# Kernel optimization log

Measured on AMD Instinct MI355X. Metric: run time of the kernel, lower is better.

The kernel has to match this reference:

```python
import jax, jax.numpy as jnp
import numpy as np

B, S, D = 2, 2048, 2048
H, KVH = 16, 4
HD = D // H  # 128


def _rope_angles(seq, head_dim):
    theta = 1.0 / (10000.0 ** (jnp.arange(0, head_dim, 2, dtype=jnp.float32) / head_dim))
    ang = jnp.arange(seq, dtype=jnp.float32)[:, None] * theta[None, :]  # [S, HD/2]
    return jnp.cos(ang), jnp.sin(ang)


def _apply_rotary(t, cos, sin):
    # t: [B, S, h, HD]; pairs are (even, odd) along last dim (view_as_complex semantics)
    tr = t[..., 0::2]
    ti = t[..., 1::2]
    c = cos[None, :, None, :]
    s = sin[None, :, None, :]
    out_r = tr * c - ti * s
    out_i = tr * s + ti * c
    return jnp.stack([out_r, out_i], axis=-1).reshape(t.shape)


def setup_inputs() -> dict:
    key = jax.random.key(0)
    ks = jax.random.split(key, 8)
    sd = 1.0 / np.sqrt(D)
    return {
        'x': jax.random.normal(ks[0], (B, S, D), dtype=jnp.float32),
        'wq': jax.random.normal(ks[1], (D, D), dtype=jnp.float32) * sd,
        'bq': jax.random.normal(ks[2], (D,), dtype=jnp.float32) * 0.01,
        'wk': jax.random.normal(ks[3], (D, KVH * HD), dtype=jnp.float32) * sd,
        'bk': jax.random.normal(ks[4], (KVH * HD,), dtype=jnp.float32) * 0.01,
        'wv': jax.random.normal(ks[5], (D, KVH * HD), dtype=jnp.float32) * sd,
        'bv': jax.random.normal(ks[6], (KVH * HD,), dtype=jnp.float32) * 0.01,
        'wo': jax.random.normal(ks[7], (D, D), dtype=jnp.float32) * sd,
    }


def reference(x, wq, bq, wk, bk, wv, bv, wo):
    b, s, d = x.shape
    q = (x @ wq + bq).reshape(b, s, H, HD)
    k = (x @ wk + bk).reshape(b, s, KVH, HD)
    v = (x @ wv + bv).reshape(b, s, KVH, HD)

    cos, sin = _rope_angles(s, HD)
    q = _apply_rotary(q, cos, sin)
    k = _apply_rotary(k, cos, sin)

    repeat = H // KVH
    k = jnp.repeat(k, repeat, axis=2)  # [B, S, H, HD]
    v = jnp.repeat(v, repeat, axis=2)

    scale = 1.0 / np.sqrt(HD)
    att_score = jnp.einsum('bqhd,bkhd->bqhk', q, k) * scale  # [B, S, H, S]
    att_weight = jax.nn.softmax(att_score, axis=-1)
    out = jnp.einsum('bqhk,bkhd->bqhd', att_weight, v)
    out = out.reshape(b, s, H * HD)
    return out @ wo
```

## Files before the change

### kernel.cpp

```cpp
#include <hip/hip_runtime.h>
#include <hip/hip_bf16.h>
#include <cstdint>

typedef __attribute__((ext_vector_type(4))) float f32x4;
typedef __attribute__((ext_vector_type(16))) float f32x16;
typedef __attribute__((ext_vector_type(8))) short bf16x8;
typedef __attribute__((ext_vector_type(4))) unsigned int u32x4;
typedef unsigned short u16;
typedef unsigned int u32;

__device__ __forceinline__ u16 f2b(float x) {
  __hip_bfloat16 h = __float2bfloat16(x);
  return *reinterpret_cast<u16*>(&h);
}

__device__ __forceinline__ u32 pk(float a, float b) {
  __hip_bfloat162 h2 = __float22bfloat162_rn(float2{a, b});
  return *reinterpret_cast<u32*>(&h2);
}

__device__ __forceinline__ void gload16(const void* g, void* l) {
  __builtin_amdgcn_global_load_lds((const __attribute__((address_space(1))) u32*)g,
                                   (__attribute__((address_space(3))) u32*)l, 16, 0, 0);
}

__device__ __forceinline__ float xmax32(float x) {
  return fmaxf(x, __shfl_xor(x, 32, 64));
}
__device__ __forceinline__ float xsum32(float x) {
  return x + __shfl_xor(x, 32, 64);
}


__global__ void cvt_f32_bf16(const float* __restrict__ in, u16* __restrict__ out, int n4) {
  int idx = (blockIdx.x * 256 + threadIdx.x);
  if (idx < n4) {
    const float4 v = *(const float4*)(in + (size_t)idx * 4);
    u16* o = out + (size_t)idx * 4;
    o[0] = f2b(v.x); o[1] = f2b(v.y); o[2] = f2b(v.z); o[3] = f2b(v.w);
  }
}

__global__ void w_transpose_cvt(const float* __restrict__ w0, const float* __restrict__ w1,
                                const float* __restrict__ w2, int b0, int b1,
                                int N0, int N1, int N2,
                                u16* __restrict__ out, int K) {
  __shared__ float tile[32][33];
  int k0 = blockIdx.x * 32, n0 = blockIdx.y * 32;
  const float* src; int srcN; int c0;
  if (n0 < b0)      { src = w0; srcN = N0; c0 = n0; }
  else if (n0 < b1) { src = w1; srcN = N1; c0 = n0 - b0; }
  else              { src = w2; srcN = N2; c0 = n0 - b1; }
  int tx = threadIdx.x & 31, ty = threadIdx.x >> 5;
#pragma unroll
  for (int j = 0; j < 32; j += 8)
    tile[ty + j][tx] = src[(size_t)(k0 + ty + j) * srcN + c0 + tx];
  __syncthreads();
#pragma unroll
  for (int j = 0; j < 32; j += 8)
    out[(size_t)(n0 + ty + j) * K + k0 + tx] = f2b(tile[tx][ty + j]);
}

__global__ void pack_bias(const float* __restrict__ bq, const float* __restrict__ bk,
                          const float* __restrict__ bv, float* __restrict__ out) {
  int i = blockIdx.x * 256 + threadIdx.x;
  if (i < 3072) out[i] = (i < 2048) ? bq[i] : ((i < 2560) ? bk[i - 2048] : bv[i - 2560]);
}

__global__ void v_transpose_cvt(const float* __restrict__ qkv, u16* __restrict__ vt) {
  __shared__ float tile[32][33];
  int s0 = blockIdx.x * 32;
  int d0 = blockIdx.y * 32;
  int z = blockIdx.z;
  int b = z >> 2, kvh = z & 3;
  int tx = threadIdx.x & 31, ty = threadIdx.x >> 5;
#pragma unroll
  for (int j = 0; j < 32; j += 8)
    tile[ty + j][tx] = qkv[((size_t)(b * 2048 + s0 + ty + j)) * 3072 + 2560 + kvh * 128 + d0 + tx];
  __syncthreads();
#pragma unroll
  for (int j = 0; j < 32; j += 8)
    vt[((size_t)z * 128 + d0 + ty + j) * 2048 + s0 + tx] = f2b(tile[tx][ty + j]);
}

__global__ void rope_cvt(const float* __restrict__ qkv, u16* __restrict__ out,
                         int lognh, int col0, float scale) {
  int idx = blockIdx.x * 256 + threadIdx.x;
  int i = idx & 63;
  int nh = 1 << lognh;
  int h = (idx >> 6) & (nh - 1);
  int bs = idx >> (6 + lognh);
  int s = bs & 2047;
  int b = bs >> 11;
  const float* src = qkv + (size_t)bs * 3072 + col0 + h * 128 + 2 * i;
  float tr = src[0], ti = src[1];
  float theta = expf(-(float)i * 0.14391156831212787f);
  float ang = (float)s * theta;
  float sv, cv;
  sincosf(ang, &sv, &cv);
  float orr = (tr * cv - ti * sv) * scale;
  float oii = (tr * sv + ti * cv) * scale;
  u16* dst = out + (((size_t)(b * nh + h) * 2048 + s) * 128 + 2 * i);
  dst[0] = f2b(orr);
  dst[1] = f2b(oii);
}

__global__ __launch_bounds__(256) void gemm_bt_bf16(
    const u16* __restrict__ A, const u16* __restrict__ Bt,
    const float* __restrict__ bias, float* __restrict__ C,
    int M, int N, int K, int gx) {
  __shared__ u16 As[128 * 32];
  __shared__ u16 Bs[128 * 32];
  const int tid = threadIdx.x;
  const int lane = tid & 63;
  const int w = tid >> 6;
  const int wr = w >> 1, wc = w & 1;
  const int nb = gridDim.x;
  const int swz = (blockIdx.x & 7) * (nb >> 3) + (blockIdx.x >> 3);
  const int m0 = (swz / gx) * 128;
  const int n0 = (swz % gx) * 128;

  f32x4 acc[4][4] = {};

  for (int k0 = 0; k0 < K; k0 += 32) {
#pragma unroll
    for (int it = 0; it < 2; ++it) {
      int c = tid + it * 256;
      int row = c >> 2;
      int off = (c & 3) * 8;
      gload16(A + (size_t)(m0 + row) * K + k0 + off, (u16*)As + w * 512 + it * 2048);
      gload16(Bt + (size_t)(n0 + row) * K + k0 + off, (u16*)Bs + w * 512 + it * 2048);
    }
    __syncthreads();
    const int col8 = (lane >> 4) * 8;
    bf16x8 a[4], bfr[4];
#pragma unroll
    for (int m = 0; m < 4; ++m)
      a[m] = *(const bf16x8*)&As[(wr * 64 + m * 16 + (lane & 15)) * 32 + col8];
#pragma unroll
    for (int n = 0; n < 4; ++n)
      bfr[n] = *(const bf16x8*)&Bs[(wc * 64 + n * 16 + (lane & 15)) * 32 + col8];
#pragma unroll
    for (int m = 0; m < 4; ++m)
#pragma unroll
      for (int n = 0; n < 4; ++n)
        acc[m][n] = __builtin_amdgcn_mfma_f32_16x16x32_bf16(a[m], bfr[n], acc[m][n], 0, 0, 0);
    __syncthreads();
  }

#pragma unroll
  for (int m = 0; m < 4; ++m) {
    int row = m0 + wr * 64 + m * 16 + ((lane >> 4) << 2);
#pragma unroll
    for (int n = 0; n < 4; ++n) {
      int col = n0 + wc * 64 + n * 16 + (lane & 15);
      float bvv = bias ? bias[col] : 0.f;
      float* cp = C + (size_t)row * N + col;
#pragma unroll
      for (int r = 0; r < 4; ++r) cp[(size_t)r * N] = acc[m][n][r] + bvv;
    }
  }
}

__global__ __launch_bounds__(128, 3) void flash_attn(
    const u16* __restrict__ Qr, const u16* __restrict__ Kr,
    const u16* __restrict__ Vt, u16* __restrict__ Att) {
  __shared__ u16 Ks[2][32 * 128];
  __shared__ u16 Vs[2][128 * 32];
  const int tid = threadIdx.x, lane = tid & 63, w = tid >> 6;
  const int lo = lane & 31, hi = lane >> 5;
  const int bid = blockIdx.x;
  const int g = bid & 7;
  const int local = bid >> 3;
  const int b = g >> 2, kvh = g & 3;
  const int h = kvh * 4 + (local & 3);
  const int q0 = (local >> 2) * 64 + w * 32;

  const char* Khead = (const char*)(Kr + (size_t)(b * 4 + kvh) * 2048 * 128);
  const char* Vhead = (const char*)(Vt + (size_t)(b * 4 + kvh) * 128 * 2048);

  bf16x8 qf[8];
  {
    const u16* qp = Qr + ((size_t)(b * 16 + h) * 2048 + q0 + lo) * 128 + hi * 8;
#pragma unroll
    for (int ds = 0; ds < 8; ++ds) qf[ds] = *(const bf16x8*)(qp + ds * 16);
  }

#define STAGE(bufi, t)                                                        \
  {                                                                           \
    _Pragma("unroll")                                                         \
    for (int it = 0; it < 4; ++it) {                                          \
      int c = it * 128 + tid;                                                 \
      int krow = c >> 4;                                                      \
      int koff = krow * 256 + ((c & 15) << 4 ^ ((krow & 7) << 4));            \
      gload16(Khead + (size_t)(t) * 8192 + koff,                              \
              (u16*)Ks[bufi] + it * 1024 + w * 512);                          \
      int vrow = c >> 2;                                                      \
      int voff = vrow * 4096 + ((c & 3) << 4 ^ (((vrow >> 1) & 3) << 4));     \
      gload16(Vhead + (size_t)(t) * 64 + voff,                                \
              (u16*)Vs[bufi] + it * 1024 + w * 512);                          \
    }                                                                         \
  }

  f32x16 o0[4] = {};
  float m_run = -3.0e38f, l_run = 0.f;
  const int swz = (lo & 7) << 4;
  const int vswz = ((lo >> 1) & 3) << 4;
  const int hi16 = hi * 16;

  STAGE(0, 0);
  __syncthreads();

  int buf = 0;
  for (int t = 0; t < 64; ++t) {
    int tn = (t < 63) ? t + 1 : 63;
    STAGE(buf ^ 1, tn);

    const char* Kb = (const char*)Ks[buf];
    const char* Vb = (const char*)Vs[buf];

    f32x16 sc = {};
    __builtin_amdgcn_s_setprio(1);
#pragma unroll
    for (int ds = 0; ds < 8; ++ds) {
      bf16x8 kf = *(const bf16x8*)(Kb + lo * 256 + ((ds * 32 + hi16) ^ swz));
      sc = __builtin_amdgcn_mfma_f32_32x32x16_bf16(kf, qf[ds], sc, 0, 0, 0);
    }
    __builtin_amdgcn_s_setprio(0);

    {
      float t0 = fmaxf(fmaxf(sc[0], sc[1]), sc[2]);
      float t1 = fmaxf(fmaxf(sc[3], sc[4]), sc[5]);
      float t2 = fmaxf(fmaxf(sc[6], sc[7]), sc[8]);
      float t3 = fmaxf(fmaxf(sc[9], sc[10]), sc[11]);
      float t4 = fmaxf(fmaxf(sc[12], sc[13]), sc[14]);
      float pmax = xmax32(fmaxf(fmaxf(fmaxf(t0, t1), t2), fmaxf(fmaxf(t3, t4), sc[15])));
      if (!__all(pmax - m_run <= 11.0f)) {
        float mnew = fmaxf(m_run, pmax);
        float rs = exp2f(m_run - mnew);
        m_run = mnew;
        l_run *= rs;
#pragma unroll
        for (int r = 0; r < 16; ++r) {
          float rsr = __shfl(rs, (r & 3) + 8 * (r >> 2) + 4 * hi, 64);
          o0[0][r] *= rsr; o0[1][r] *= rsr; o0[2][r] *= rsr; o0[3][r] *= rsr;
        }
      }
      float lsum = 0.f;
#pragma unroll
      for (int r = 0; r < 16; ++r) { float p = exp2f(sc[r] - m_run); sc[r] = p; lsum += p; }
      l_run += xsum32(lsum);
    }

    bf16x8 pa0, pa1;
    {
      u32 a0 = pk(sc[0], sc[1]),   a1 = pk(sc[2], sc[3]);
      u32 b0 = pk(sc[4], sc[5]),   b1 = pk(sc[6], sc[7]);
      u32 t0 = hi ? a0 : b0, t1 = hi ? a1 : b1;
      u32 r0 = __shfl_xor(t0, 32, 64), r1 = __shfl_xor(t1, 32, 64);
      u32x4 w0;
      w0[0] = hi ? r0 : a0; w0[1] = hi ? r1 : a1;
      w0[2] = hi ? b0 : r0; w0[3] = hi ? b1 : r1;
      pa0 = __builtin_bit_cast(bf16x8, w0);
      u32 c0 = pk(sc[8], sc[9]),   c1 = pk(sc[10], sc[11]);
      u32 d0 = pk(sc[12], sc[13]), d1 = pk(sc[14], sc[15]);
      u32 t2 = hi ? c0 : d0, t3 = hi ? c1 : d1;
      u32 r2 = __shfl_xor(t2, 32, 64), r3 = __shfl_xor(t3, 32, 64);
      u32x4 w1;
      w1[0] = hi ? r2 : c0; w1[1] = hi ? r3 : c1;
      w1[2] = hi ? d0 : r2; w1[3] = hi ? d1 : r3;
      pa1 = __builtin_bit_cast(bf16x8, w1);
    }

    __builtin_amdgcn_s_setprio(1);
#pragma unroll
    for (int n = 0; n < 4; ++n) {
      const char* vrb = Vb + (n * 32 + lo) * 64;
      bf16x8 vb0 = *(const bf16x8*)(vrb + ((0  + hi16) ^ vswz));
      bf16x8 vb1 = *(const bf16x8*)(vrb + ((32 + hi16) ^ vswz));
      o0[n] = __builtin_amdgcn_mfma_f32_32x32x16_bf16(pa0, vb0, o0[n], 0, 0, 0);
      o0[n] = __builtin_amdgcn_mfma_f32_32x32x16_bf16(pa1, vb1, o0[n], 0, 0, 0);
    }
    __builtin_amdgcn_s_setprio(0);

    __syncthreads();
    buf ^= 1;
  }

  float inv = 1.0f / l_run;
  size_t rowbase = (size_t)(b * 2048 + q0);
#pragma unroll
  for (int r = 0; r < 16; ++r) {
    int rr = (r & 3) + 8 * (r >> 2) + 4 * hi;
    float invr = __shfl(inv, rr, 64);
    u16* op = Att + (rowbase + rr) * 2048 + h * 128 + lo;
    op[0]  = f2b(o0[0][r] * invr);
    op[32] = f2b(o0[1][r] * invr);
    op[64] = f2b(o0[2][r] * invr);
    op[96] = f2b(o0[3][r] * invr);
  }
}


extern "C" void kernel_launch(void* const* d_in, const int* in_sizes, int n_in,
                              void* d_out, int out_size, void* d_ws, size_t ws_size,
                              hipStream_t stream) {
  const float* x  = (const float*)d_in[0];
  const float* wq = (const float*)d_in[1];
  const float* bq = (const float*)d_in[2];
  const float* wk = (const float*)d_in[3];
  const float* bk = (const float*)d_in[4];
  const float* wv = (const float*)d_in[5];
  const float* bv = (const float*)d_in[6];
  const float* wo = (const float*)d_in[7];
  float* out = (float*)d_out;
  char* ws = (char*)d_ws;

  u16*   x_bf   = (u16*)  (ws + 0);
  u16*   att    = (u16*)  (ws + 0);
  u16*   wqkv_t = (u16*)  (ws + 16777216);
  u16*   wo_t   = (u16*)  (ws + 29360128);
  float* biasq  = (float*)(ws + 37748736);
  float* qkv    = (float*)(ws + 37761024);
  u16*   q_r    = (u16*)  (ws + 88092672);
  u16*   k_r    = (u16*)  (ws + 104869888);
  u16*   v_t    = (u16*)  (ws + 109064192);

  cvt_f32_bf16<<<8192, 256, 0, stream>>>(x, x_bf, 2097152);
  w_transpose_cvt<<<dim3(64, 96), 256, 0, stream>>>(wq, wk, wv, 2048, 2560,
                                                    2048, 512, 512, wqkv_t, 2048);
  w_transpose_cvt<<<dim3(64, 64), 256, 0, stream>>>(wo, wo, wo, 2048, 2560,
                                                    2048, 2048, 2048, wo_t, 2048);
  pack_bias<<<12, 256, 0, stream>>>(bq, bk, bv, biasq);

  gemm_bt_bf16<<<768, 256, 0, stream>>>(x_bf, wqkv_t, biasq, qkv, 4096, 3072, 2048, 24);

  rope_cvt<<<16384, 256, 0, stream>>>(qkv, q_r, 4, 0, 0.12751743871465216f);
  rope_cvt<<<4096, 256, 0, stream>>>(qkv, k_r, 2, 2048, 1.0f);
  v_transpose_cvt<<<dim3(64, 4, 8), 256, 0, stream>>>(qkv, v_t);

  flash_attn<<<1024, 128, 0, stream>>>(q_r, k_r, v_t, att);

  gemm_bt_bf16<<<512, 256, 0, stream>>>(att, wo_t, nullptr, out, 4096, 2048, 2048, 16);
}
```

Before: 305.3 us.

## Triple-buffer flash attention K/V staging and compute row sums via MFMA

Moves the flash attention kernel from double to triple buffering of K/V tiles. A partial vmcnt wait plus a barrier lets two tiles stay in flight, and the next stage is issued after compute rather than before it. The softmax row sum is now taken by MFMAs against a ones vector, replacing the scalar sums and cross-lane shuffles. The block index mapping changes to a 3D grid that no longer groups blocks by KV head, and launch bounds drop to 2 blocks per CU. This adds LDS use and accumulator registers and may reduce L2 reuse of K/V across neighbouring blocks.

```diff
diff --git a/kernel.cpp b/kernel.cpp
--- a/kernel.cpp
+++ b/kernel.cpp
@@ -26,9 +26,6 @@
 
 __device__ __forceinline__ float xmax32(float x) {
   return fmaxf(x, __shfl_xor(x, 32, 64));
-}
-__device__ __forceinline__ float xsum32(float x) {
-  return x + __shfl_xor(x, 32, 64);
 }
 
 
@@ -162,19 +159,16 @@
   }
 }
 
-__global__ __launch_bounds__(128, 3) void flash_attn(
+__global__ __launch_bounds__(128, 2) void flash_attn(
     const u16* __restrict__ Qr, const u16* __restrict__ Kr,
     const u16* __restrict__ Vt, u16* __restrict__ Att) {
-  __shared__ u16 Ks[2][32 * 128];
-  __shared__ u16 Vs[2][128 * 32];
+  __shared__ u16 Ks[3][32 * 128];
+  __shared__ u16 Vs[3][128 * 32];
   const int tid = threadIdx.x, lane = tid & 63, w = tid >> 6;
   const int lo = lane & 31, hi = lane >> 5;
-  const int bid = blockIdx.x;
-  const int g = bid & 7;
-  const int local = bid >> 3;
-  const int b = g >> 2, kvh = g & 3;
-  const int h = kvh * 4 + (local & 3);
-  const int q0 = (local >> 2) * 64 + w * 32;
+  const int q0 = blockIdx.x * 64 + w * 32;
+  const int h = blockIdx.y, b = blockIdx.z;
+  const int kvh = h >> 2;
 
   const char* Khead = (const char*)(Kr + (size_t)(b * 4 + kvh) * 2048 * 128);
   const char* Vhead = (const char*)(Vt + (size_t)(b * 4 + kvh) * 128 * 2048);
@@ -202,22 +196,29 @@
     }                                                                         \
   }
 
+#define WAITBAR() asm volatile("s_waitcnt vmcnt(8)\n\ts_barrier" ::: "memory")
+
   f32x16 o0[4] = {};
-  float m_run = -3.0e38f, l_run = 0.f;
+  f32x16 l_acc = {};
+  float m_run = -3.0e38f;
   const int swz = (lo & 7) << 4;
   const int vswz = ((lo >> 1) & 3) << 4;
   const int hi16 = hi * 16;
 
+  bf16x8 ones8;
+  {
+    u32x4 ov; ov[0] = 0x3f803f80u; ov[1] = 0x3f803f80u; ov[2] = 0x3f803f80u; ov[3] = 0x3f803f80u;
+    ones8 = __builtin_bit_cast(bf16x8, ov);
+  }
+
   STAGE(0, 0);
-  __syncthreads();
-
-  int buf = 0;
+  STAGE(1, 1);
+  WAITBAR();
+
+  int cur = 0;
   for (int t = 0; t < 64; ++t) {
-    int tn = (t < 63) ? t + 1 : 63;
-    STAGE(buf ^ 1, tn);
-
-    const char* Kb = (const char*)Ks[buf];
-    const char* Vb = (const char*)Vs[buf];
+    const char* Kb = (const char*)Ks[cur];
+    const char* Vb = (const char*)Vs[cur];
 
     f32x16 sc = {};
     __builtin_amdgcn_s_setprio(1);
@@ -239,17 +240,15 @@
         float mnew = fmaxf(m_run, pmax);
         float rs = exp2f(m_run - mnew);
         m_run = mnew;
-        l_run *= rs;
 #pragma unroll
         for (int r = 0; r < 16; ++r) {
           float rsr = __shfl(rs, (r & 3) + 8 * (r >> 2) + 4 * hi, 64);
           o0[0][r] *= rsr; o0[1][r] *= rsr; o0[2][r] *= rsr; o0[3][r] *= rsr;
+          l_acc[r] *= rsr;
         }
       }
-      float lsum = 0.f;
-#pragma unroll
-      for (int r = 0; r < 16; ++r) { float p = exp2f(sc[r] - m_run); sc[r] = p; lsum += p; }
-      l_run += xsum32(lsum);
+#pragma unroll
+      for (int r = 0; r < 16; ++r) sc[r] = exp2f(sc[r] - m_run);
     }
 
     bf16x8 pa0, pa1;
@@ -273,6 +272,8 @@
     }
 
     __builtin_amdgcn_s_setprio(1);
+    l_acc = __builtin_amdgcn_mfma_f32_32x32x16_bf16(pa0, ones8, l_acc, 0, 0, 0);
+    l_acc = __builtin_amdgcn_mfma_f32_32x32x16_bf16(pa1, ones8, l_acc, 0, 0, 0);
 #pragma unroll
     for (int n = 0; n < 4; ++n) {
       const char* vrb = Vb + (n * 32 + lo) * 64;
@@ -283,16 +284,19 @@
     }
     __builtin_amdgcn_s_setprio(0);
 
-    __syncthreads();
-    buf ^= 1;
-  }
-
-  float inv = 1.0f / l_run;
+    int tn = (t + 2 < 64) ? t + 2 : 63;
+    int nxt = cur + 2; if (nxt >= 3) nxt -= 3;
+    STAGE(nxt, tn);
+    WAITBAR();
+
+    cur = cur + 1; if (cur == 3) cur = 0;
+  }
+
   size_t rowbase = (size_t)(b * 2048 + q0);
 #pragma unroll
   for (int r = 0; r < 16; ++r) {
     int rr = (r & 3) + 8 * (r >> 2) + 4 * hi;
-    float invr = __shfl(inv, rr, 64);
+    float invr = 1.0f / l_acc[r];
     u16* op = Att + (rowbase + rr) * 2048 + h * 128 + lo;
     op[0]  = f2b(o0[0][r] * invr);
     op[32] = f2b(o0[1][r] * invr);
@@ -339,7 +343,7 @@
   rope_cvt<<<4096, 256, 0, stream>>>(qkv, k_r, 2, 2048, 1.0f);
   v_transpose_cvt<<<dim3(64, 4, 8), 256, 0, stream>>>(qkv, v_t);
 
-  flash_attn<<<1024, 128, 0, stream>>>(q_r, k_r, v_t, att);
+  flash_attn<<<dim3(32, 16, 2), 128, 0, stream>>>(q_r, k_r, v_t, att);
 
   gemm_bt_bf16<<<512, 256, 0, stream>>>(att, wo_t, nullptr, out, 4096, 2048, 2048, 16);
 }
```

Result: slower. 337.8 us (+10.6%).
